# Kernel tuning notes

Hardware: AMD Instinct MI355X
Metric: run time of the kernel (lower is better)

The kernel has to match this reference:

```python
import jax, jax.numpy as jnp
import numpy as np
from jax import lax

INPUT, HIDDEN, LAYERS = 256, 512, 2
B, T = 128, 512


def setup_inputs() -> dict:
    key = jax.random.key(0)
    ks = jax.random.split(key, 8)
    s_in = 1.0 / np.sqrt(HIDDEN)
    x = jax.random.normal(ks[0], (B, T, INPUT), dtype=jnp.float32)
    # PyTorch LSTM layout: W_ih [4H, in], W_hh [4H, H], gate order (i, f, g, o).
    w_ih0 = jax.random.uniform(ks[1], (4 * HIDDEN, INPUT), jnp.float32, -s_in, s_in)
    w_hh0 = jax.random.uniform(ks[2], (4 * HIDDEN, HIDDEN), jnp.float32, -s_in, s_in)
    b0 = jax.random.uniform(ks[3], (4 * HIDDEN,), jnp.float32, -s_in, s_in)  # b_ih + b_hh combined
    w_ih1 = jax.random.uniform(ks[4], (4 * HIDDEN, HIDDEN), jnp.float32, -s_in, s_in)
    w_hh1 = jax.random.uniform(ks[5], (4 * HIDDEN, HIDDEN), jnp.float32, -s_in, s_in)
    b1 = jax.random.uniform(ks[6], (4 * HIDDEN,), jnp.float32, -s_in, s_in)
    # fc: xavier_uniform weight, bias init to constant 30 per init_weights()
    lim = np.sqrt(6.0 / (HIDDEN + 1))
    fc_w = jax.random.uniform(ks[7], (1, HIDDEN), jnp.float32, -lim, lim)
    fc_b = jnp.full((1,), 30.0, dtype=jnp.float32)
    return {"x": x, "w_ih0": w_ih0, "w_hh0": w_hh0, "b0": b0,
            "w_ih1": w_ih1, "w_hh1": w_hh1, "b1": b1,
            "fc_w": fc_w, "fc_b": fc_b}


def _lstm_layer(x, w_ih, w_hh, b):
    # x: [B, T, D] -> outputs [B, T, H], final hidden [B, H]
    Bb, Tt = x.shape[0], x.shape[1]
    H = w_hh.shape[1]
    # Precompute input projection for all timesteps (big GEMM).
    xg = jnp.einsum('btd,gd->btg', x, w_ih) + b  # [B, T, 4H]
    h0 = jnp.zeros((Bb, H), dtype=x.dtype)
    c0 = jnp.zeros((Bb, H), dtype=x.dtype)

    def step(carry, xt):
        h, c = carry
        g = xt + h @ w_hh.T  # [B, 4H]
        i, f, gg, o = jnp.split(g, 4, axis=-1)
        c = jax.nn.sigmoid(f) * c + jax.nn.sigmoid(i) * jnp.tanh(gg)
        h = jax.nn.sigmoid(o) * jnp.tanh(c)
        return (h, c), h

    (hT, cT), ys = lax.scan(step, (h0, c0), xg.transpose(1, 0, 2))
    return ys.transpose(1, 0, 2), hT


def reference(x, w_ih0, w_hh0, b0, w_ih1, w_hh1, b1, fc_w, fc_b):
    y0, h0 = _lstm_layer(x, w_ih0, w_hh0, b0)
    y1, h1 = _lstm_layer(y0, w_ih1, w_hh1, b1)
    hn = jnp.concatenate([h0, h1], axis=0)  # hn.view(-1, H): [L*B, H]
    return hn @ fc_w.T + fc_b  # [L*B, 1]
```

## Files before the change

### kernel.cpp

```cpp
#include <hip/hip_runtime.h>
#include <stdint.h>


using s16x8 = __attribute__((ext_vector_type(8))) short;
using f32x4 = __attribute__((ext_vector_type(4))) float;
typedef unsigned long long ull;

#define WSB1_OFF 1572864
#define HB0_OFF  3670016
#define HB1_OFF  3801088
#define TAGS_BYTE_OFF 7864320

__device__ __forceinline__ float bf2f(unsigned short u) {
    unsigned v = ((unsigned)u) << 16;
    return __builtin_bit_cast(float, v);
}
__device__ __forceinline__ unsigned short f2bf(float f) {
    unsigned x = __builtin_bit_cast(unsigned, f);
    x += 0x7FFFu + ((x >> 16) & 1u);
    return (unsigned short)(x >> 16);
}
__device__ __forceinline__ float sigm(float x) { return 1.f / (1.f + __expf(-x)); }
__device__ __forceinline__ float tanhc(float x) {
    x = fminf(15.f, fmaxf(-15.f, x));
    float e = __expf(-2.f * x);
    return (1.f - e) / (1.f + e);
}

__device__ __forceinline__ void store_frag(unsigned short* dst, int n, int kc, int KT,
                                           const float* src) {
    s16x8 v;
#pragma unroll
    for (int e = 0; e < 8; ++e) v[e] = (short)f2bf(src[e]);
    int gate = n >> 9, hid = n & 511;
    int rt = hid >> 5;
    int w  = (hid >> 3) & 3;
    int t  = gate >> 1;
    int lo = (gate & 1) * 8 + (hid & 7);
    int tileIdx = w * 2 + t;
    int kt = kc >> 2, q = kc & 3;
    int lane = q * 16 + lo;
    size_t off = ((((size_t)rt * 8 + tileIdx) * KT + kt) * 64 + lane) * 8;
    *(s16x8*)(dst + off) = v;
}

__global__ void k_prep(const float* __restrict__ wih0, const float* __restrict__ whh0,
                       const float* __restrict__ wih1, const float* __restrict__ whh1,
                       unsigned short* __restrict__ wsB0, unsigned short* __restrict__ wsB1,
                       unsigned short* __restrict__ hb0, unsigned short* __restrict__ hb1,
                       unsigned* __restrict__ tags) {
    int idx = blockIdx.x * 256 + threadIdx.x;
    if (idx < 196608) {
        int n = idx / 96, kc = idx - n * 96;
        int k = kc * 8;
        const float* src = (k < 256) ? (wih0 + (size_t)n * 256 + k)
                                     : (whh0 + (size_t)n * 512 + (k - 256));
        store_frag(wsB0, n, kc, 24, src);
    } else if (idx < 458752) {
        int j = idx - 196608;
        int n = j >> 7, kc = j & 127;
        int k = kc * 8;
        const float* src = (k < 512) ? (wih1 + (size_t)n * 512 + k)
                                     : (whh1 + (size_t)n * 512 + (k - 512));
        store_frag(wsB1, n, kc, 32, src);
    } else {
        int z = idx - 458752;
        if (z < 8192) {
            ull* p = (ull*)(hb0 + 65536 + (size_t)z * 8);
            p[0] = 0ull; p[1] = 0ull;
        } else if (z < 16384) {
            ull* p = (ull*)(hb1 + (size_t)(z - 8192) * 8);
            p[0] = 0ull; p[1] = 0ull;
        } else if (z < 16640) {
            tags[(size_t)(z - 16384) * 32] = 0u;
        }
    }
}

template <int LAYER, int KT>
__device__ __forceinline__ void run_layer(const float* __restrict__ x,
                                          const unsigned short* __restrict__ wsB,
                                          unsigned short* hsrc0,
                                          unsigned short* hself,
                                          unsigned* tags,
                                          unsigned* mytag,
                                          float bv0, float bv1,
                                          int g, int rt, int w, int lane, int tid,
                                          char* At) {
    constexpr int PITCH = (LAYER == 0) ? 1600 : 2112;
    constexpr int KTX   = 8;
    const int lm = lane & 15, lq = lane >> 4;

    s16x8 bfr0[KT], bfr1[KT];
    {
        const unsigned short* base = wsB + (((size_t)rt * 8 + 2 * w) * KT) * 512;
#pragma unroll
        for (int kt = 0; kt < KT; ++kt) {
            bfr0[kt] = *(const s16x8*)(base + ((size_t)kt * 64 + lane) * 8);
            bfr1[kt] = *(const s16x8*)(base + (((size_t)KT + kt) * 64 + lane) * 8);
        }
    }

    float cst[4] = {0.f, 0.f, 0.f, 0.f};

    f32x4 xa[2], xb[2];
    int xrow[2], xch[2];
    if (LAYER == 0) {
#pragma unroll
        for (int i = 0; i < 2; ++i) {
            int task = tid + i * 256;
            xrow[i] = task >> 5; xch[i] = task & 31;
            const float* src = x + ((size_t)(g * 16 + xrow[i]) * 512) * 256 + xch[i] * 8;
            xa[i] = *(const f32x4*)(src);
            xb[i] = *(const f32x4*)(src + 4);
        }
    }

#pragma unroll 1
    for (int s = 0; s <= 512; ++s) {
        const bool active = LAYER ? (s >= 1) : (s < 512);
        const int pr = (s + 1) & 1;
        const int pw = s & 1;

        f32x4 acc0 = {0.f, 0.f, 0.f, 0.f}, acc1 = {0.f, 0.f, 0.f, 0.f};
        const char* ap = At + lm * PITCH + lq * 16;

        if (LAYER == 0 && active) {
#pragma unroll
            for (int i = 0; i < 2; ++i) {
                s16x8 v;
#pragma unroll
                for (int e = 0; e < 4; ++e) { v[e] = (short)f2bf(xa[i][e]); v[4 + e] = (short)f2bf(xb[i][e]); }
                *(s16x8*)(At + xrow[i] * PITCH + xch[i] * 16) = v;
            }
            if (s + 1 < 512) {
#pragma unroll
                for (int i = 0; i < 2; ++i) {
                    const float* src = x + ((size_t)(g * 16 + xrow[i]) * 512 + (s + 1)) * 256 + xch[i] * 8;
                    xa[i] = *(const f32x4*)(src);
                    xb[i] = *(const f32x4*)(src + 4);
                }
            }
            __syncthreads();

#pragma unroll
            for (int kt = 0; kt < KTX; ++kt) {
                s16x8 a = *(const s16x8*)(ap + kt * 64);
                acc0 = __builtin_amdgcn_mfma_f32_16x16x32_bf16(a, bfr0[kt], acc0, 0, 0, 0);
                acc1 = __builtin_amdgcn_mfma_f32_16x16x32_bf16(a, bfr1[kt], acc1, 0, 0, 0);
            }
        }

        if (tid < 32) {
            unsigned* tp = tags + (size_t)tid * 32;
            while (__hip_atomic_load(tp, __ATOMIC_RELAXED, __HIP_MEMORY_SCOPE_SYSTEM) < (unsigned)s)
                __builtin_amdgcn_s_sleep(1);
        }
        __syncthreads();

        if (active) {
            if (LAYER == 0) {
#pragma unroll
                for (int i = 0; i < 4; ++i) {
                    int task = tid + i * 256;
                    int row = task >> 6, c8 = task & 63;
                    const ull* sp = (const ull*)(hsrc0 + (size_t)(pr * 128 + g * 16 + row) * 512 + c8 * 8);
                    ull v0 = __hip_atomic_load(sp,     __ATOMIC_RELAXED, __HIP_MEMORY_SCOPE_SYSTEM);
                    ull v1 = __hip_atomic_load(sp + 1, __ATOMIC_RELAXED, __HIP_MEMORY_SCOPE_SYSTEM);
                    ull* d = (ull*)(At + row * PITCH + 512 + c8 * 16);
                    d[0] = v0; d[1] = v1;
                }
            } else {
#pragma unroll
                for (int i = 0; i < 8; ++i) {
                    int task = tid + i * 256;
                    int row = task >> 7, c8 = task & 127;
                    const unsigned short* sp = (c8 < 64)
                        ? (hsrc0 + (size_t)(pr * 128 + g * 16 + row) * 512 + c8 * 8)
                        : (hself + (size_t)(pr * 128 + g * 16 + row) * 512 + (c8 - 64) * 8);
                    ull v0 = __hip_atomic_load((const ull*)sp,     __ATOMIC_RELAXED, __HIP_MEMORY_SCOPE_SYSTEM);
                    ull v1 = __hip_atomic_load((const ull*)sp + 1, __ATOMIC_RELAXED, __HIP_MEMORY_SCOPE_SYSTEM);
                    ull* d = (ull*)(At + row * PITCH + c8 * 16);
                    d[0] = v0; d[1] = v1;
                }
            }
            __syncthreads();

#pragma unroll
            for (int kt = (LAYER == 0 ? KTX : 0); kt < KT; ++kt) {
                s16x8 a = *(const s16x8*)(ap + kt * 64);
                acc0 = __builtin_amdgcn_mfma_f32_16x16x32_bf16(a, bfr0[kt], acc0, 0, 0, 0);
                acc1 = __builtin_amdgcn_mfma_f32_16x16x32_bf16(a, bfr1[kt], acc1, 0, 0, 0);
            }

            const bool hi = (lm & 8) != 0;
            float hv[4];
#pragma unroll
            for (int r = 0; r < 4; ++r) {
                float a0 = acc0[r] + bv0;
                float a1 = acc1[r] + bv1;
                float a0x = __shfl_xor(a0, 8, 16);
                float a1x = __shfl_xor(a1, 8, 16);
                float iv = hi ? a0x : a0;
                float fv = hi ? a0  : a0x;
                float gv = hi ? a1x : a1;
                float ov = hi ? a1  : a1x;
                float cn = sigm(fv) * cst[r] + sigm(iv) * tanhc(gv);
                cst[r] = cn;
                hv[r] = sigm(ov) * tanhc(cn);
            }

            ull packed = 0;
#pragma unroll
            for (int r = 0; r < 4; ++r)
                packed |= ((ull)f2bf(hv[r])) << (16 * r);
            ull outp = 0;
            const int rp = (lm >> 1) & 3;
#pragma unroll
            for (int e = 0; e < 4; ++e) {
                ull got = __shfl(packed, (lm & 1) * 4 + e, 16);
                ull val = (got >> (16 * rp)) & 0xFFFFull;
                outp |= val << (16 * e);
            }
            if (lm < 8) {
                int brow = lq * 4 + (lm >> 1);
                size_t off = (size_t)(pw * 128 + g * 16 + brow) * 512
                           + rt * 32 + w * 8 + (lm & 1) * 4;
                __hip_atomic_store((ull*)(hself + off), outp,
                                   __ATOMIC_RELAXED, __HIP_MEMORY_SCOPE_SYSTEM);
            }
        }

        __syncthreads();
        if (tid == 0)
            __hip_atomic_store(mytag, (unsigned)(s + 1),
                               __ATOMIC_RELAXED, __HIP_MEMORY_SCOPE_SYSTEM);
    }
}

__launch_bounds__(256, 1)
__global__ void k_lstm(const float* __restrict__ x,
                       const float* __restrict__ b0,
                       const float* __restrict__ b1,
                       const unsigned short* __restrict__ wsB0,
                       const unsigned short* __restrict__ wsB1,
                       unsigned short* hb0, unsigned short* hb1,
                       unsigned* tags) {
    __shared__ __align__(16) char Atile[16 * 2112];

    const int tid = threadIdx.x;
    const int g = blockIdx.x & 7, sub = blockIdx.x >> 3;
    const int layer = sub >> 4, rt = sub & 15;
    const int w = tid >> 6, lane = tid & 63;
    const int lm = lane & 15;

    unsigned* gtags = tags + (size_t)g * 32 * 32;
    unsigned* mytag = gtags + (size_t)(layer * 16 + rt) * 32;

    const float* bias = layer ? b1 : b0;
    const int jsub = rt * 32 + w * 8 + (lm & 7);
    const int G0 = (lm & 8) ? 1 : 0;
    const float bv0 = bias[G0 * 512 + jsub];
    const float bv1 = bias[(G0 + 2) * 512 + jsub];

    if (layer == 0)
        run_layer<0, 24>(x, wsB0, hb0, hb0, gtags, mytag, bv0, bv1,
                         g, rt, w, lane, tid, Atile);
    else
        run_layer<1, 32>(x, wsB1, hb0, hb1, gtags, mytag, bv0, bv1,
                         g, rt, w, lane, tid, Atile);
}

__global__ void k_fc(const unsigned short* __restrict__ hb0,
                     const unsigned short* __restrict__ hb1,
                     const float* __restrict__ fcw, const float* __restrict__ fcb,
                     float* __restrict__ out) {
    int i = blockIdx.x, lane = threadIdx.x;
    const unsigned short* hrow = (i < 128) ? (hb0 + (size_t)(128 + i) * 512)
                                           : (hb1 + (size_t)(i - 128) * 512);
    float ssum = 0.f;
    int j0 = lane * 8;
#pragma unroll
    for (int e = 0; e < 8; ++e) ssum += bf2f(hrow[j0 + e]) * fcw[j0 + e];
#pragma unroll
    for (int off2 = 32; off2 > 0; off2 >>= 1) ssum += __shfl_down(ssum, off2);
    if (lane == 0) out[i] = ssum + fcb[0];
}

extern "C" void kernel_launch(void* const* d_in, const int* in_sizes, int n_in,
                              void* d_out, int out_size, void* d_ws, size_t ws_size,
                              hipStream_t stream) {
    const float* x    = (const float*)d_in[0];
    const float* wih0 = (const float*)d_in[1];
    const float* whh0 = (const float*)d_in[2];
    const float* b0   = (const float*)d_in[3];
    const float* wih1 = (const float*)d_in[4];
    const float* whh1 = (const float*)d_in[5];
    const float* b1   = (const float*)d_in[6];
    const float* fcw  = (const float*)d_in[7];
    const float* fcb  = (const float*)d_in[8];

    unsigned short* wsB0 = (unsigned short*)d_ws;
    unsigned short* wsB1 = wsB0 + WSB1_OFF;
    unsigned short* hb0  = wsB0 + HB0_OFF;
    unsigned short* hb1  = wsB0 + HB1_OFF;
    unsigned* tags = (unsigned*)((char*)d_ws + TAGS_BYTE_OFF);
    float* out = (float*)d_out;

    k_prep<<<dim3(1857), dim3(256), 0, stream>>>(wih0, whh0, wih1, whh1,
                                                 wsB0, wsB1, hb0, hb1, tags);

    k_lstm<<<dim3(256), dim3(256), 0, stream>>>(x, b0, b1, wsB0, wsB1, hb0, hb1, tags);

    k_fc<<<dim3(256), dim3(64), 0, stream>>>(hb0, hb1, fcw, fcb, out);
}
```

Before: 2.855 ms.

## Split tag waits per layer so recurrent wait overlaps cross-layer input work

The single wait on all 32 tag flags each timestep is replaced by finer waits on the 16 tags of the relevant producer group. Layer 1 now waits only on its own layer's tags first, computes the recurrent half of the matmul, then waits on layer 0's tags for the input half. Layer 0 waits on its own tags before loading h and on layer 1's tags only before overwriting its output buffer. This shrinks the lockstep coupling between the two layer pipelines so they can drift and overlap, at the cost of extra __syncthreads and more complex buffer-reuse ordering that must still be race-free.

```diff
diff --git a/kernel.cpp b/kernel.cpp
--- a/kernel.cpp
+++ b/kernel.cpp
@@ -25,6 +25,9 @@
     x = fminf(15.f, fmaxf(-15.f, x));
     float e = __expf(-2.f * x);
     return (1.f - e) / (1.f + e);
+}
+__device__ __forceinline__ unsigned tagld(const unsigned* p) {
+    return __hip_atomic_load(p, __ATOMIC_RELAXED, __HIP_MEMORY_SCOPE_SYSTEM);
 }
 
 __device__ __forceinline__ void store_frag(unsigned short* dst, int n, int kc, int KT,
@@ -89,6 +92,7 @@
                                           char* At) {
     constexpr int PITCH = (LAYER == 0) ? 1600 : 2112;
     constexpr int KTX   = 8;
+    constexpr int KTY   = 16;
     const int lm = lane & 15, lq = lane >> 4;
 
     s16x8 bfr0[KT], bfr1[KT];
@@ -122,44 +126,41 @@
         const int pr = (s + 1) & 1;
         const int pw = s & 1;
 
-        f32x4 acc0 = {0.f, 0.f, 0.f, 0.f}, acc1 = {0.f, 0.f, 0.f, 0.f};
-        const char* ap = At + lm * PITCH + lq * 16;
-
-        if (LAYER == 0 && active) {
-#pragma unroll
-            for (int i = 0; i < 2; ++i) {
-                s16x8 v;
-#pragma unroll
-                for (int e = 0; e < 4; ++e) { v[e] = (short)f2bf(xa[i][e]); v[4 + e] = (short)f2bf(xb[i][e]); }
-                *(s16x8*)(At + xrow[i] * PITCH + xch[i] * 16) = v;
-            }
-            if (s + 1 < 512) {
+        if (active) {
+            f32x4 acc0 = {0.f, 0.f, 0.f, 0.f}, acc1 = {0.f, 0.f, 0.f, 0.f};
+            const char* ap = At + lm * PITCH + lq * 16;
+
+            if (LAYER == 0) {
 #pragma unroll
                 for (int i = 0; i < 2; ++i) {
-                    const float* src = x + ((size_t)(g * 16 + xrow[i]) * 512 + (s + 1)) * 256 + xch[i] * 8;
-                    xa[i] = *(const f32x4*)(src);
-                    xb[i] = *(const f32x4*)(src + 4);
-                }
-            }
-            __syncthreads();
-
-#pragma unroll
-            for (int kt = 0; kt < KTX; ++kt) {
-                s16x8 a = *(const s16x8*)(ap + kt * 64);
-                acc0 = __builtin_amdgcn_mfma_f32_16x16x32_bf16(a, bfr0[kt], acc0, 0, 0, 0);
-                acc1 = __builtin_amdgcn_mfma_f32_16x16x32_bf16(a, bfr1[kt], acc1, 0, 0, 0);
-            }
-        }
-
-        if (tid < 32) {
-            unsigned* tp = tags + (size_t)tid * 32;
-            while (__hip_atomic_load(tp, __ATOMIC_RELAXED, __HIP_MEMORY_SCOPE_SYSTEM) < (unsigned)s)
-                __builtin_amdgcn_s_sleep(1);
-        }
-        __syncthreads();
-
-        if (active) {
-            if (LAYER == 0) {
+                    s16x8 v;
+#pragma unroll
+                    for (int e = 0; e < 4; ++e) { v[e] = (short)f2bf(xa[i][e]); v[4 + e] = (short)f2bf(xb[i][e]); }
+                    *(s16x8*)(At + xrow[i] * PITCH + xch[i] * 16) = v;
+                }
+                if (s + 1 < 512) {
+#pragma unroll
+                    for (int i = 0; i < 2; ++i) {
+                        const float* src = x + ((size_t)(g * 16 + xrow[i]) * 512 + (s + 1)) * 256 + xch[i] * 8;
+                        xa[i] = *(const f32x4*)(src);
+                        xb[i] = *(const f32x4*)(src + 4);
+                    }
+                }
+                __syncthreads();
+
+#pragma unroll
+                for (int kt = 0; kt < KTX; ++kt) {
+                    s16x8 a = *(const s16x8*)(ap + kt * 64);
+                    acc0 = __builtin_amdgcn_mfma_f32_16x16x32_bf16(a, bfr0[kt], acc0, 0, 0, 0);
+                    acc1 = __builtin_amdgcn_mfma_f32_16x16x32_bf16(a, bfr1[kt], acc1, 0, 0, 0);
+                }
+
+                if (tid < 16) {
+                    unsigned* tp = tags + (size_t)tid * 32;
+                    while (tagld(tp) < (unsigned)s) __builtin_amdgcn_s_sleep(1);
+                }
+                __syncthreads();
+
 #pragma unroll
                 for (int i = 0; i < 4; ++i) {
                     int task = tid + i * 256;
@@ -170,27 +171,64 @@
                     ull* d = (ull*)(At + row * PITCH + 512 + c8 * 16);
                     d[0] = v0; d[1] = v1;
                 }
+                __syncthreads();
+
+#pragma unroll
+                for (int kt = KTX; kt < KT; ++kt) {
+                    s16x8 a = *(const s16x8*)(ap + kt * 64);
+                    acc0 = __builtin_amdgcn_mfma_f32_16x16x32_bf16(a, bfr0[kt], acc0, 0, 0, 0);
+                    acc1 = __builtin_amdgcn_mfma_f32_16x16x32_bf16(a, bfr1[kt], acc1, 0, 0, 0);
+                }
             } else {
-#pragma unroll
-                for (int i = 0; i < 8; ++i) {
+                if (tid < 16) {
+                    unsigned* tp = tags + (size_t)(16 + tid) * 32;
+                    while (tagld(tp) < (unsigned)s) __builtin_amdgcn_s_sleep(1);
+                }
+                __syncthreads();
+
+#pragma unroll
+                for (int i = 0; i < 4; ++i) {
                     int task = tid + i * 256;
-                    int row = task >> 7, c8 = task & 127;
-                    const unsigned short* sp = (c8 < 64)
-                        ? (hsrc0 + (size_t)(pr * 128 + g * 16 + row) * 512 + c8 * 8)
-                        : (hself + (size_t)(pr * 128 + g * 16 + row) * 512 + (c8 - 64) * 8);
-                    ull v0 = __hip_atomic_load((const ull*)sp,     __ATOMIC_RELAXED, __HIP_MEMORY_SCOPE_SYSTEM);
-                    ull v1 = __hip_atomic_load((const ull*)sp + 1, __ATOMIC_RELAXED, __HIP_MEMORY_SCOPE_SYSTEM);
+                    int row = task >> 6, c8 = task & 63;
+                    const ull* sp = (const ull*)(hself + (size_t)(pr * 128 + g * 16 + row) * 512 + c8 * 8);
+                    ull v0 = __hip_atomic_load(sp,     __ATOMIC_RELAXED, __HIP_MEMORY_SCOPE_SYSTEM);
+                    ull v1 = __hip_atomic_load(sp + 1, __ATOMIC_RELAXED, __HIP_MEMORY_SCOPE_SYSTEM);
+                    ull* d = (ull*)(At + row * PITCH + 1024 + c8 * 16);
+                    d[0] = v0; d[1] = v1;
+                }
+                __syncthreads();
+
+#pragma unroll
+                for (int kt = KTY; kt < KT; ++kt) {
+                    s16x8 a = *(const s16x8*)(ap + kt * 64);
+                    acc0 = __builtin_amdgcn_mfma_f32_16x16x32_bf16(a, bfr0[kt], acc0, 0, 0, 0);
+                    acc1 = __builtin_amdgcn_mfma_f32_16x16x32_bf16(a, bfr1[kt], acc1, 0, 0, 0);
+                }
+
+                if (tid < 16) {
+                    unsigned* tp = tags + (size_t)tid * 32;
+                    while (tagld(tp) < (unsigned)s) __builtin_amdgcn_s_sleep(1);
+                }
+                __syncthreads();
+
+#pragma unroll
+                for (int i = 0; i < 4; ++i) {
+                    int task = tid + i * 256;
+                    int row = task >> 6, c8 = task & 63;
+                    const ull* sp = (const ull*)(hsrc0 + (size_t)(pr * 128 + g * 16 + row) * 512 + c8 * 8);
+                    ull v0 = __hip_atomic_load(sp,     __ATOMIC_RELAXED, __HIP_MEMORY_SCOPE_SYSTEM);
+                    ull v1 = __hip_atomic_load(sp + 1, __ATOMIC_RELAXED, __HIP_MEMORY_SCOPE_SYSTEM);
                     ull* d = (ull*)(At + row * PITCH + c8 * 16);
                     d[0] = v0; d[1] = v1;
                 }
-            }
-            __syncthreads();
-
-#pragma unroll
-            for (int kt = (LAYER == 0 ? KTX : 0); kt < KT; ++kt) {
-                s16x8 a = *(const s16x8*)(ap + kt * 64);
-                acc0 = __builtin_amdgcn_mfma_f32_16x16x32_bf16(a, bfr0[kt], acc0, 0, 0, 0);
-                acc1 = __builtin_amdgcn_mfma_f32_16x16x32_bf16(a, bfr1[kt], acc1, 0, 0, 0);
+                __syncthreads();
+
+#pragma unroll
+                for (int kt = 0; kt < KTY; ++kt) {
+                    s16x8 a = *(const s16x8*)(ap + kt * 64);
+                    acc0 = __builtin_amdgcn_mfma_f32_16x16x32_bf16(a, bfr0[kt], acc0, 0, 0, 0);
+                    acc1 = __builtin_amdgcn_mfma_f32_16x16x32_bf16(a, bfr1[kt], acc1, 0, 0, 0);
+                }
             }
 
             const bool hi = (lm & 8) != 0;
@@ -210,6 +248,14 @@
                 hv[r] = sigm(ov) * tanhc(cn);
             }
 
+            if (LAYER == 0) {
+                if (tid < 16) {
+                    unsigned* tp = tags + (size_t)(16 + tid) * 32;
+                    while (tagld(tp) < (unsigned)s) __builtin_amdgcn_s_sleep(1);
+                }
+                __syncthreads();
+            }
+
             ull packed = 0;
 #pragma unroll
             for (int r = 0; r < 4; ++r)
```

Result: faster. 2.656 ms (-7.0%).
